# Performance work log

Measured on AMD Instinct MI355X. Metric: run time of the kernel, lower is better.

Reference implementation:

```python
import jax, jax.numpy as jnp
import numpy as np

N_NODES = 20000
N_EDGES = 320000
N_GRAPHS = 32
C = 256
L = 4
IN_DIM = 739
EDGE_DIM = 2 * C + 6
LN_EPS = 1e-5


def _layernorm(x, g, b):
    mu = jnp.mean(x, axis=-1, keepdims=True)
    var = jnp.mean(jnp.square(x - mu), axis=-1, keepdims=True)
    return (x - mu) * jax.lax.rsqrt(var + LN_EPS) * g + b


def setup_inputs() -> dict:
    key = jax.random.key(0)
    ks = jax.random.split(key, 20)
    d = {}
    d["x"] = jax.random.normal(ks[0], (N_NODES, IN_DIM), jnp.float32)
    d["x_pos"] = jax.random.normal(ks[1], (N_NODES, 3), jnp.float32)
    d["edge_index"] = jax.random.randint(ks[2], (2, N_EDGES), 0, N_NODES, jnp.int32)
    d["batch"] = jnp.sort(jax.random.randint(ks[3], (N_NODES,), 0, N_GRAPHS, jnp.int32))
    s = 0.02
    d["dense_w"] = jax.random.normal(ks[4], (IN_DIM, C), jnp.float32) * s
    d["dense_b"] = jnp.zeros((C,), jnp.float32)
    d["d1_w"] = jax.random.normal(ks[5], (L, C, C), jnp.float32) * s
    d["d1_b"] = jnp.zeros((L, C), jnp.float32)
    d["ln1_g"] = jnp.ones((L, EDGE_DIM), jnp.float32)
    d["ln1_b"] = jnp.zeros((L, EDGE_DIM), jnp.float32)
    d["w1_w"] = jax.random.normal(ks[6], (L, EDGE_DIM, 4), jnp.float32) * s
    d["w1_b"] = jnp.zeros((L, 4), jnp.float32)
    d["ln2_g"] = jnp.ones((L, 4), jnp.float32)
    d["ln2_b"] = jnp.zeros((L, 4), jnp.float32)
    d["w2_w"] = jax.random.normal(ks[7], (L, 4, 1), jnp.float32) * s
    d["w2_b"] = jnp.zeros((L, 1), jnp.float32)
    d["d2_w"] = jax.random.normal(ks[8], (L, C, C), jnp.float32) * s
    d["d2_b"] = jnp.zeros((L, C), jnp.float32)
    d["head_w"] = jax.random.normal(ks[9], (C, 1), jnp.float32) * s
    d["head_b"] = jnp.zeros((1,), jnp.float32)
    return d


def reference(x, x_pos, edge_index, batch, dense_w, dense_b, d1_w, d1_b,
              ln1_g, ln1_b, w1_w, w1_b, ln2_g, ln2_b, w2_w, w2_b,
              d2_w, d2_b, head_w, head_b):
    n = x.shape[0]
    src, dst = edge_index[0], edge_index[1]
    h = x @ dense_w + dense_b  # [N, C]
    for l in range(d1_w.shape[0]):
        # message: dense1 -> GELU (dropout is identity in eval)
        m = jax.nn.gelu(h @ d1_w[l] + d1_b[l], approximate=False)  # [N, C]
        sx = m[src]                                                # [E, C]
        # edge-MLP input: [src_x, dst_x, src_pos, dst_pos]
        e = jnp.concatenate([sx, m[dst], x_pos[src], x_pos[dst]], axis=-1)  # [E, 2C+6]
        e = _layernorm(e, ln1_g[l], ln1_b[l])
        e = jax.nn.gelu(e @ w1_w[l] + w1_b[l], approximate=False)  # [E, 4]
        e = _layernorm(e, ln2_g[l], ln2_b[l])
        w = jax.nn.sigmoid(e @ w2_w[l] + w2_b[l])                  # [E, 1]
        agg = jax.ops.segment_sum(sx * w, dst, num_segments=n)     # [N, C]
        # update: dense2 -> GELU
        h = jax.nn.gelu(agg @ d2_w[l] + d2_b[l], approximate=False)
    # global mean pool over graphs
    sums = jax.ops.segment_sum(h, batch, num_segments=N_GRAPHS)           # [G, C]
    cnts = jax.ops.segment_sum(jnp.ones((n, 1), h.dtype), batch, num_segments=N_GRAPHS)
    pooled = sums / jnp.maximum(cnts, 1.0)
    return pooled @ head_w + head_b  # [G, 1]
```

## Files before the change

kernel.cpp:

```cpp
#include <hip/hip_runtime.h>
#include <math.h>

#define N_NODES 20000
#define N_EDGES 320000
#define N_GRAPHS 32
#define CDIM 256
#define IN_DIMV 739
#define KPAD_DENSE 768
#define ED_DIM 518
#define NLAYERS 4
#define LN_EPS 1e-5f
#define SCAN_BLOCKS ((N_NODES + 255) / 256)

typedef _Float16 f16x8 __attribute__((ext_vector_type(8)));
typedef _Float16 f16x4 __attribute__((ext_vector_type(4)));
typedef float f32x4 __attribute__((ext_vector_type(4)));

__device__ __forceinline__ float gelu_exact(float x) {
    return 0.5f * x * (1.f + erff(x * 0.7071067811865475f));
}

__device__ __forceinline__ void gll16(const void* g, void* l) {
    __builtin_amdgcn_global_load_lds((const __attribute__((address_space(1))) void*)g,
                                     (__attribute__((address_space(3))) void*)l, 16, 0, 0);
}

__global__ __launch_bounds__(256)
void prep_all(const float* __restrict__ ln1_g, const float* __restrict__ ln1_b,
              const float* __restrict__ w1_w, float* __restrict__ cw,
              float* __restrict__ SgSb,
              const float* __restrict__ dense_w, _Float16* __restrict__ wt_dense,
              const float* __restrict__ d1_w, const float* __restrict__ d2_w,
              _Float16* __restrict__ wt_sq, int* __restrict__ deg,
              float* __restrict__ sdot,
              const float* __restrict__ x, _Float16* __restrict__ xh) {
    __shared__ float smem[2048 + 64];
    int b = blockIdx.x, tid = threadIdx.x;
    if (b < 79) {
        int i = b * 256 + tid;
        if (i < N_NODES) deg[i] = 0;
    } else if (b < 83) {
        int l = b - 79;
        float sg[4] = {0, 0, 0, 0}, sb[4] = {0, 0, 0, 0};
        for (int i = tid; i < ED_DIM; i += 256) {
            float g = ln1_g[l * ED_DIM + i];
            float bb = ln1_b[l * ED_DIM + i];
            float4 w = *(const float4*)&w1_w[(size_t)(l * ED_DIM + i) * 4];
            float4 c = make_float4(g * w.x, g * w.y, g * w.z, g * w.w);
            *(float4*)&cw[(size_t)(l * ED_DIM + i) * 4] = c;
            sg[0] += c.x; sg[1] += c.y; sg[2] += c.z; sg[3] += c.w;
            sb[0] += bb * w.x; sb[1] += bb * w.y; sb[2] += bb * w.z; sb[3] += bb * w.w;
        }
        for (int c = 0; c < 4; c++) { smem[tid * 8 + c] = sg[c]; smem[tid * 8 + 4 + c] = sb[c]; }
        __syncthreads();
        for (int s = 128; s > 0; s >>= 1) {
            if (tid < s)
                for (int c = 0; c < 8; c++) smem[tid * 8 + c] += smem[(tid + s) * 8 + c];
            __syncthreads();
        }
        if (tid < 8) SgSb[l * 8 + tid] = smem[tid];
    } else if (b < 275) {
        int q = b - 83;
        int kt = q >> 3, nt = q & 7;
        int i = tid >> 5, j = tid & 31;
        float* T = smem;
#pragma unroll
        for (int ii = 0; ii < 4; ii++) {
            int k = kt * 32 + i + ii * 8;
            T[(i + ii * 8) * 33 + j] = (k < IN_DIMV) ? dense_w[(size_t)k * 256 + nt * 32 + j] : 0.f;
        }
        __syncthreads();
#pragma unroll
        for (int ii = 0; ii < 4; ii++) {
            int n = nt * 32 + i + ii * 8;
            wt_dense[(size_t)n * KPAD_DENSE + kt * 32 + j] = (_Float16)T[j * 33 + i + ii * 8];
        }
    } else if (b < 787) {
        int q = b - 275;
        int z = q >> 6, kt = (q >> 3) & 7, nt = q & 7;
        const float* W = (z < 4) ? d1_w + (size_t)z * 65536 : d2_w + (size_t)(z - 4) * 65536;
        _Float16* O = wt_sq + (size_t)z * 65536;
        int i = tid >> 5, j = tid & 31;
        float* T = smem;
#pragma unroll
        for (int ii = 0; ii < 4; ii++)
            T[(i + ii * 8) * 33 + j] = W[(size_t)(kt * 32 + i + ii * 8) * 256 + nt * 32 + j];
        __syncthreads();
#pragma unroll
        for (int ii = 0; ii < 4; ii++)
            O[(size_t)(nt * 32 + i + ii * 8) * 256 + kt * 32 + j] = (_Float16)T[j * 33 + i + ii * 8];
    } else if (b < 866) {
        int i = (b - 787) * 256 + tid;
        if (i < N_NODES) sdot[i] = 0.f;
    } else {
        const int cb = b - 866;
        const int stride = 2048 * 256;
        const int nquads = (N_NODES * IN_DIMV) / 4;
        for (int q = cb * 256 + tid; q < nquads; q += stride) {
            float4 v = ((const float4*)x)[q];
            int base = q * 4;
            float vv[4] = {v.x, v.y, v.z, v.w};
#pragma unroll
            for (int e = 0; e < 4; ++e) {
                int idx = base + e;
                int row = idx / IN_DIMV;
                int col = idx - row * IN_DIMV;
                xh[row * KPAD_DENSE + col] = (_Float16)vv[e];
            }
        }
        const int npad = N_NODES * (KPAD_DENSE - IN_DIMV);
        for (int p = cb * 256 + tid; p < npad; p += stride) {
            int row = p / (KPAD_DENSE - IN_DIMV);
            int col = IN_DIMV + (p - row * (KPAD_DENSE - IN_DIMV));
            xh[row * KPAD_DENSE + col] = (_Float16)0.f;
        }
    }
}

__global__ void hist_gstart_kernel(const int* __restrict__ ei, const int* __restrict__ batch,
                                   int* __restrict__ deg, int* __restrict__ gstart) {
    int e = blockIdx.x * 256 + threadIdx.x;
    if (e < N_EDGES) atomicAdd(&deg[ei[N_EDGES + e]], 1);
    if (e < N_NODES) {
        int b = batch[e];
        int bprev = (e == 0) ? -1 : batch[e - 1];
        for (int g = bprev + 1; g <= b; g++) gstart[g] = e;
        if (e == N_NODES - 1)
            for (int g = b + 1; g <= N_GRAPHS; g++) gstart[g] = N_NODES;
    }
}

__global__ __launch_bounds__(256)
void scan1_kernel(const int* __restrict__ deg, int* __restrict__ bsum) {
    __shared__ int red[256];
    int t = threadIdx.x;
    int i = blockIdx.x * 256 + t;
    red[t] = (i < N_NODES) ? deg[i] : 0;
    __syncthreads();
    for (int s = 128; s > 0; s >>= 1) {
        if (t < s) red[t] += red[t + s];
        __syncthreads();
    }
    if (t == 0) bsum[blockIdx.x] = red[0];
}

__global__ __launch_bounds__(128)
void scan2_kernel(const int* __restrict__ bsum, int* __restrict__ boff) {
    __shared__ int s[128];
    int t = threadIdx.x;
    int v = (t < SCAN_BLOCKS) ? bsum[t] : 0;
    s[t] = v;
    __syncthreads();
    for (int off = 1; off < 128; off <<= 1) {
        int o = (t >= off) ? s[t - off] : 0;
        __syncthreads();
        s[t] += o;
        __syncthreads();
    }
    if (t < SCAN_BLOCKS) boff[t] = s[t] - v;
}

__global__ __launch_bounds__(256)
void scan3_kernel(const int* __restrict__ deg, const int* __restrict__ boff,
                  int* __restrict__ row_start, int* __restrict__ cursor) {
    __shared__ int s[256];
    int t = threadIdx.x;
    int i = blockIdx.x * 256 + t;
    int v = (i < N_NODES) ? deg[i] : 0;
    s[t] = v;
    __syncthreads();
    for (int off = 1; off < 256; off <<= 1) {
        int o = (t >= off) ? s[t - off] : 0;
        __syncthreads();
        s[t] += o;
        __syncthreads();
    }
    int base = boff[blockIdx.x];
    int excl = base + s[t] - v;
    if (i < N_NODES) {
        row_start[i] = excl;
        cursor[i] = excl;
    }
    if (i == N_NODES - 1) row_start[N_NODES] = base + s[t];
}

__global__ void scatter_kernel(const int* __restrict__ ei, int* __restrict__ cursor,
                               int* __restrict__ csr_src, int* __restrict__ slot) {
    int e = blockIdx.x * 256 + threadIdx.x;
    if (e < N_EDGES) {
        int d = ei[N_EDGES + e];
        int pos = atomicAdd(&cursor[d], 1);
        csr_src[pos] = ei[e];
        slot[e] = pos;
    }
}

template <int KSTEPS, int NBUF, bool GELU_ACT, bool DOT, bool SUMPART>
__global__ __launch_bounds__(256)
void gemm_v6(const _Float16* __restrict__ A, const _Float16* __restrict__ Bt,
             const float* __restrict__ bias, _Float16* __restrict__ C,
             const float* __restrict__ head_w, float* __restrict__ sdot,
             const float* __restrict__ cw, float* __restrict__ nsp) {
    constexpr int KDIM = KSTEPS * 64;
    __shared__ __align__(16) _Float16 Bs[NBUF * 128 * 64];
    __shared__ __align__(16) _Float16 As[NBUF * 64 * 64];

    const int tid = threadIdx.x;
    const int row0 = blockIdx.x * 64;
    const int col0 = blockIdx.y * 128;
    const int wave = tid >> 6, lane = tid & 63;
    const int quad = lane >> 4, lrow = lane & 15;
    const int wrow = wave >> 1, wcol = wave & 1;

    const int sr = tid >> 3;
    const int scb = (tid & 7) << 4;
    const int srcCb = scb ^ ((sr & 7) << 4);

    const char* bsrc[4];
#pragma unroll
    for (int i = 0; i < 4; ++i)
        bsrc[i] = (const char*)Bt + (size_t)(col0 + i * 32 + sr) * (KDIM * 2) + srcCb;
    char* const bdst = (char*)&Bs[0] + tid * 16;

    const char* asrc[2];
    char* const adst = (char*)&As[0] + tid * 16;
#pragma unroll
    for (int i = 0; i < 2; ++i) {
        int ar = row0 + i * 32 + sr;
        ar = (ar < N_NODES) ? ar : (N_NODES - 1);
        asrc[i] = (const char*)A + (size_t)ar * (KDIM * 2) + srcCb;
    }

    const int swz = ((lrow & 7) << 4) ^ (quad << 4);
    const int aro0 = (wrow * 32 + lrow) * 128;
    const int aro1 = aro0 + 2048;
    int bro[4];
#pragma unroll
    for (int t = 0; t < 4; ++t) bro[t] = (wcol * 64 + t * 16 + lrow) * 128;

    f32x4 acc[2][4];
#pragma unroll
    for (int i = 0; i < 2; ++i)
#pragma unroll
        for (int t = 0; t < 4; ++t) acc[i][t] = (f32x4){0.f, 0.f, 0.f, 0.f};

    auto stage = [&](int j) {
        const int kb = j * 128;
        const int b3 = (j % NBUF) * 16384;
        const int a3 = (j % NBUF) * 8192;
#pragma unroll
        for (int i = 0; i < 4; ++i) gll16(bsrc[i] + kb, bdst + b3 + i * 4096);
#pragma unroll
        for (int i = 0; i < 2; ++i) gll16(asrc[i] + kb, adst + a3 + i * 4096);
    };

    auto compute = [&](int k) {
        const char* pa = (const char*)&As[0] + (k % NBUF) * 8192;
        const char* pb = (const char*)&Bs[0] + (k % NBUF) * 16384;
        if constexpr (NBUF == 3) __builtin_amdgcn_s_setprio(1);
#pragma unroll
        for (int h = 0; h < 2; ++h) {
            const int cbs = (h << 6) ^ swz;
            f16x8 af0 = *(const f16x8*)(pa + aro0 + cbs);
            f16x8 af1 = *(const f16x8*)(pa + aro1 + cbs);
#pragma unroll
            for (int t = 0; t < 4; ++t) {
                f16x8 bf = *(const f16x8*)(pb + bro[t] + cbs);
                acc[0][t] = __builtin_amdgcn_mfma_f32_16x16x32_f16(af0, bf, acc[0][t], 0, 0, 0);
                acc[1][t] = __builtin_amdgcn_mfma_f32_16x16x32_f16(af1, bf, acc[1][t], 0, 0, 0);
            }
        }
        if constexpr (NBUF == 3) __builtin_amdgcn_s_setprio(0);
    };

    stage(0);
    if constexpr (NBUF == 3) {
        if (KSTEPS > 1) stage(1);
        asm volatile("s_waitcnt vmcnt(6)" ::: "memory");
        __builtin_amdgcn_sched_barrier(0);
        __builtin_amdgcn_s_barrier();
        __builtin_amdgcn_sched_barrier(0);
    } else {
        __syncthreads();
    }

#pragma unroll
    for (int k = 0; k < KSTEPS; ++k) {
        const int nxt = k + NBUF - 1;
        if (nxt < KSTEPS) stage(nxt);
        compute(k);
        if (k + 1 < KSTEPS) {
            if constexpr (NBUF == 3) {
                if (k + 2 < KSTEPS)
                    asm volatile("s_waitcnt vmcnt(6) lgkmcnt(0)" ::: "memory");
                else
                    asm volatile("s_waitcnt vmcnt(0) lgkmcnt(0)" ::: "memory");
                __builtin_amdgcn_sched_barrier(0);
                __builtin_amdgcn_s_barrier();
                __builtin_amdgcn_sched_barrier(0);
            } else {
                __syncthreads();
            }
        }
    }

    const int orow = row0 + wrow * 32 + quad * 4;
    const int ocolb = col0 + wcol * 64 + lrow;
    if constexpr (DOT) {
        float dp0[4] = {0.f, 0.f, 0.f, 0.f}, dp1[4] = {0.f, 0.f, 0.f, 0.f};
#pragma unroll
        for (int t = 0; t < 4; ++t) {
            const int col = ocolb + t * 16;
            const float hw = head_w[col];
            const float bv = bias[col];
#pragma unroll
            for (int r = 0; r < 4; ++r) {
                dp0[r] += gelu_exact(acc[0][t][r] + bv) * hw;
                dp1[r] += gelu_exact(acc[1][t][r] + bv) * hw;
            }
        }
#pragma unroll
        for (int r = 0; r < 4; ++r) {
#pragma unroll
            for (int off = 1; off < 16; off <<= 1) {
                dp0[r] += __shfl_xor(dp0[r], off, 64);
                dp1[r] += __shfl_xor(dp1[r], off, 64);
            }
        }
        if (lrow == 0) {
#pragma unroll
            for (int r = 0; r < 4; ++r) {
                if (orow + r < N_NODES) atomicAdd(&sdot[orow + r], dp0[r]);
                if (orow + 16 + r < N_NODES) atomicAdd(&sdot[orow + 16 + r], dp1[r]);
            }
        }
    } else if constexpr (SUMPART) {
        float4 c0v[4], c1v[4];
        float bv[4];
#pragma unroll
        for (int t = 0; t < 4; ++t) {
            const int col = ocolb + t * 16;
            c0v[t] = *(const float4*)&cw[(size_t)col * 4];
            c1v[t] = *(const float4*)&cw[(size_t)(256 + col) * 4];
            bv[t] = bias[col];
        }
        const int part = blockIdx.y * 2 + wcol;
        float* const npbase = nsp + (size_t)part * N_NODES * 12;
#pragma unroll
        for (int h = 0; h < 2; ++h) {
#pragma unroll
            for (int r = 0; r < 4; ++r) {
                const int row = orow + h * 16 + r;
                float p1x = 0.f, p1y = 0.f, p1z = 0.f, p1w = 0.f;
                float p2x = 0.f, p2y = 0.f, p2z = 0.f, p2w = 0.f;
                float q1 = 0.f, q2 = 0.f;
#pragma unroll
                for (int t = 0; t < 4; ++t) {
                    float v = gelu_exact(acc[h][t][r] + bv[t]);
                    _Float16 hv = (_Float16)v;
                    if (row < N_NODES) C[(size_t)row * 256 + (ocolb + t * 16)] = hv;
                    float av = (float)hv;
                    p1x += av * c0v[t].x; p1y += av * c0v[t].y;
                    p1z += av * c0v[t].z; p1w += av * c0v[t].w;
                    p2x += av * c1v[t].x; p2y += av * c1v[t].y;
                    p2z += av * c1v[t].z; p2w += av * c1v[t].w;
                    q1 += av; q2 += av * av;
                }
#pragma unroll
                for (int off = 1; off < 16; off <<= 1) {
                    p1x += __shfl_xor(p1x, off, 64); p1y += __shfl_xor(p1y, off, 64);
                    p1z += __shfl_xor(p1z, off, 64); p1w += __shfl_xor(p1w, off, 64);
                    p2x += __shfl_xor(p2x, off, 64); p2y += __shfl_xor(p2y, off, 64);
                    p2z += __shfl_xor(p2z, off, 64); p2w += __shfl_xor(p2w, off, 64);
                    q1 += __shfl_xor(q1, off, 64); q2 += __shfl_xor(q2, off, 64);
                }
                if (lrow == 0 && row < N_NODES) {
                    float* p = npbase + (size_t)row * 12;
                    *(float4*)p = make_float4(p1x, p1y, p1z, p1w);
                    *(float4*)(p + 4) = make_float4(p2x, p2y, p2z, p2w);
                    p[8] = q1;
                    p[9] = q2;
                }
            }
        }
    } else {
#pragma unroll
        for (int t = 0; t < 4; ++t) {
            const int col = ocolb + t * 16;
            const float bv = bias[col];
#pragma unroll
            for (int r = 0; r < 4; ++r) {
                float v0 = acc[0][t][r] + bv;
                float v1 = acc[1][t][r] + bv;
                if constexpr (GELU_ACT) { v0 = gelu_exact(v0); v1 = gelu_exact(v1); }
                if (orow + r < N_NODES)
                    C[(size_t)(orow + r) * 256 + col] = (_Float16)v0;
                if (orow + 16 + r < N_NODES)
                    C[(size_t)(orow + 16 + r) * 256 + col] = (_Float16)v1;
            }
        }
    }
}

__global__ __launch_bounds__(256)
void combine_ns_kernel(const float* __restrict__ nsp, float* __restrict__ ns) {
    int i = blockIdx.x * 256 + threadIdx.x;
    const int n4 = N_NODES * 3;
    if (i >= n4) return;
    float4 a = ((const float4*)nsp)[i];
    float4 b = ((const float4*)nsp)[i + n4];
    float4 c = ((const float4*)nsp)[i + 2 * n4];
    float4 d = ((const float4*)nsp)[i + 3 * n4];
    ((float4*)ns)[i] = make_float4(a.x + b.x + c.x + d.x, a.y + b.y + c.y + d.y,
                                   a.z + b.z + c.z + d.z, a.w + b.w + c.w + d.w);
}

__global__ __launch_bounds__(256)
void edge_weight_kernel(const float* __restrict__ ns, const float* __restrict__ x_pos,
                        const int* __restrict__ ei, const float* __restrict__ cw,
                        const float* __restrict__ SgSb, const float* __restrict__ w1_b,
                        const float* __restrict__ ln2_g, const float* __restrict__ ln2_b,
                        const float* __restrict__ w2_w, const float* __restrict__ w2_b,
                        const int* __restrict__ slot, float* __restrict__ w_csr) {
    int e = blockIdx.x * 256 + threadIdx.x;
    if (e >= N_EDGES) return;
    int s = ei[e], d = ei[N_EDGES + e];
    const float* nss = &ns[(size_t)s * 12];
    const float* nsd = &ns[(size_t)d * 12];
    float4 p1 = *(const float4*)nss;
    float4 p2 = *(const float4*)(nsd + 4);
    float S1 = nss[8] + nsd[8];
    float S2 = nss[9] + nsd[9];
    float D[4] = {p1.x + p2.x, p1.y + p2.y, p1.z + p2.z, p1.w + p2.w};
    float ps[6];
    ps[0] = x_pos[(size_t)s * 3 + 0];
    ps[1] = x_pos[(size_t)s * 3 + 1];
    ps[2] = x_pos[(size_t)s * 3 + 2];
    ps[3] = x_pos[(size_t)d * 3 + 0];
    ps[4] = x_pos[(size_t)d * 3 + 1];
    ps[5] = x_pos[(size_t)d * 3 + 2];
#pragma unroll
    for (int k = 0; k < 6; k++) {
        S1 += ps[k];
        S2 += ps[k] * ps[k];
        float4 c = *(const float4*)&cw[(size_t)(512 + k) * 4];
        D[0] += ps[k] * c.x; D[1] += ps[k] * c.y; D[2] += ps[k] * c.z; D[3] += ps[k] * c.w;
    }
    const float inv = 1.f / 518.f;
    float mu = S1 * inv;
    float var = fmaf(-mu, mu, S2 * inv);
    float rstd = rsqrtf(var + LN_EPS);
    float t[4];
#pragma unroll
    for (int c = 0; c < 4; c++)
        t[c] = gelu_exact(rstd * (D[c] - mu * SgSb[c]) + SgSb[4 + c] + w1_b[c]);
    float mu2 = 0.25f * (t[0] + t[1] + t[2] + t[3]);
    float var2 = 0.25f * ((t[0] - mu2) * (t[0] - mu2) + (t[1] - mu2) * (t[1] - mu2) +
                          (t[2] - mu2) * (t[2] - mu2) + (t[3] - mu2) * (t[3] - mu2));
    float r2 = rsqrtf(var2 + LN_EPS);
    float z = w2_b[0];
#pragma unroll
    for (int c = 0; c < 4; c++)
        z += ((t[c] - mu2) * r2 * ln2_g[c] + ln2_b[c]) * w2_w[c];
    w_csr[slot[e]] = 1.f / (1.f + expf(-z));
}

__global__ __launch_bounds__(256)
void agg_kernel(const _Float16* __restrict__ m, const int* __restrict__ csr_src,
                const float* __restrict__ w_csr, const int* __restrict__ row_start,
                _Float16* __restrict__ agg) {
    int n = blockIdx.x * 4 + (threadIdx.x >> 6);
    if (n >= N_NODES) return;
    int lane = threadIdx.x & 63;
    int beg = row_start[n], end = row_start[n + 1];
    float a0 = 0.f, a1 = 0.f, a2 = 0.f, a3 = 0.f;
    int j = beg;
    for (; j + 8 <= end; j += 8) {
        int si[8];
        float wi[8];
#pragma unroll
        for (int u = 0; u < 8; u++) { si[u] = csr_src[j + u]; wi[u] = w_csr[j + u]; }
        f16x4 v[8];
#pragma unroll
        for (int u = 0; u < 8; u++) v[u] = *(const f16x4*)&m[(size_t)si[u] * CDIM + lane * 4];
#pragma unroll
        for (int u = 0; u < 8; u++) {
            a0 = fmaf(wi[u], (float)v[u][0], a0);
            a1 = fmaf(wi[u], (float)v[u][1], a1);
            a2 = fmaf(wi[u], (float)v[u][2], a2);
            a3 = fmaf(wi[u], (float)v[u][3], a3);
        }
    }
    for (; j < end; j++) {
        int s = csr_src[j];
        float w = w_csr[j];
        f16x4 v = *(const f16x4*)&m[(size_t)s * CDIM + lane * 4];
        a0 = fmaf(w, (float)v[0], a0);
        a1 = fmaf(w, (float)v[1], a1);
        a2 = fmaf(w, (float)v[2], a2);
        a3 = fmaf(w, (float)v[3], a3);
    }
    f16x4 o;
    o[0] = (_Float16)a0; o[1] = (_Float16)a1; o[2] = (_Float16)a2; o[3] = (_Float16)a3;
    *(f16x4*)&agg[(size_t)n * CDIM + lane * 4] = o;
}

__global__ __launch_bounds__(256)
void final_head_kernel(const float* __restrict__ sdot, const int* __restrict__ gstart,
                       const float* __restrict__ head_b, float* __restrict__ out) {
    int g = blockIdx.x;
    int t = threadIdx.x;
    int beg = gstart[g], end = gstart[g + 1];
    float s = 0.f;
    for (int i = beg + t; i < end; i += 256) s += sdot[i];
    __shared__ float red[256];
    red[t] = s;
    __syncthreads();
    for (int k = 128; k > 0; k >>= 1) {
        if (t < k) red[t] += red[t + k];
        __syncthreads();
    }
    if (t == 0) out[g] = red[0] / fmaxf((float)(end - beg), 1.f) + head_b[0];
}

extern "C" void kernel_launch(void* const* d_in, const int* in_sizes, int n_in,
                              void* d_out, int out_size, void* d_ws, size_t ws_size,
                              hipStream_t stream) {
    const float* x       = (const float*)d_in[0];
    const float* x_pos   = (const float*)d_in[1];
    const int*   ei      = (const int*)d_in[2];
    const int*   batch   = (const int*)d_in[3];
    const float* dense_w = (const float*)d_in[4];
    const float* dense_b = (const float*)d_in[5];
    const float* d1_w    = (const float*)d_in[6];
    const float* d1_b    = (const float*)d_in[7];
    const float* ln1_g   = (const float*)d_in[8];
    const float* ln1_b   = (const float*)d_in[9];
    const float* w1_w    = (const float*)d_in[10];
    const float* w1_b    = (const float*)d_in[11];
    const float* ln2_g   = (const float*)d_in[12];
    const float* ln2_b   = (const float*)d_in[13];
    const float* w2_w    = (const float*)d_in[14];
    const float* w2_b    = (const float*)d_in[15];
    const float* d2_w    = (const float*)d_in[16];
    const float* d2_b    = (const float*)d_in[17];
    const float* head_w  = (const float*)d_in[18];
    const float* head_b  = (const float*)d_in[19];
    float* out = (float*)d_out;

    _Float16* hbuf0 = (_Float16*)d_ws;
    _Float16* hbuf1 = hbuf0 + (size_t)N_NODES * CDIM;
    _Float16* wt_dense = hbuf1 + (size_t)N_NODES * CDIM;
    _Float16* wt_sq    = wt_dense + (size_t)256 * KPAD_DENSE;
    _Float16* x_h      = wt_sq + (size_t)8 * 256 * 256;
    float* cw    = (float*)(x_h + (size_t)N_NODES * KPAD_DENSE);
    float* SgSb  = cw + (size_t)NLAYERS * ED_DIM * 4;
    float* ns    = SgSb + NLAYERS * 8;
    float* nsp   = ns + (size_t)N_NODES * 12;
    float* sdot  = nsp + (size_t)4 * N_NODES * 12;
    float* w_csr = sdot + N_NODES;
    int* gstart    = (int*)(w_csr + N_EDGES);
    int* deg       = gstart + N_GRAPHS + 1;
    int* row_start = deg + N_NODES;
    int* cursor    = row_start + N_NODES + 1;
    int* csr_src   = cursor + N_NODES;
    int* slot      = csr_src + N_EDGES;
    int* bsum      = slot + N_EDGES;
    int* boff      = bsum + SCAN_BLOCKS;

    prep_all<<<2914, 256, 0, stream>>>(ln1_g, ln1_b, w1_w, cw, SgSb,
                                       dense_w, wt_dense, d1_w, d2_w, wt_sq, deg,
                                       sdot, x, x_h);

    hist_gstart_kernel<<<(N_EDGES + 255) / 256, 256, 0, stream>>>(ei, batch, deg, gstart);
    scan1_kernel<<<SCAN_BLOCKS, 256, 0, stream>>>(deg, bsum);
    scan2_kernel<<<1, 128, 0, stream>>>(bsum, boff);
    scan3_kernel<<<SCAN_BLOCKS, 256, 0, stream>>>(deg, boff, row_start, cursor);
    scatter_kernel<<<(N_EDGES + 255) / 256, 256, 0, stream>>>(ei, cursor, csr_src, slot);

    const dim3 G2((N_NODES + 63) / 64, 2);
    gemm_v6<12, 3, false, false, false><<<G2, 256, 0, stream>>>(
        x_h, wt_dense, dense_b, hbuf0, nullptr, nullptr, nullptr, nullptr);

    _Float16* h = hbuf0;
    _Float16* other = hbuf1;
    for (int l = 0; l < NLAYERS; l++) {
        gemm_v6<4, 2, true, false, true><<<G2, 256, 0, stream>>>(
            h, wt_sq + (size_t)l * 65536, d1_b + l * CDIM, other, nullptr, nullptr,
            cw + (size_t)l * ED_DIM * 4, nsp);
        combine_ns_kernel<<<(N_NODES * 3 + 255) / 256, 256, 0, stream>>>(nsp, ns);
        edge_weight_kernel<<<(N_EDGES + 255) / 256, 256, 0, stream>>>(
            ns, x_pos, ei, cw + (size_t)l * ED_DIM * 4, SgSb + l * 8, w1_b + l * 4,
            ln2_g + l * 4, ln2_b + l * 4, w2_w + l * 4, w2_b + l, slot, w_csr);
        agg_kernel<<<(N_NODES + 3) / 4, 256, 0, stream>>>(other, csr_src, w_csr, row_start, h);
        if (l < NLAYERS - 1) {
            gemm_v6<4, 2, true, false, false><<<G2, 256, 0, stream>>>(
                h, wt_sq + (size_t)(4 + l) * 65536, d2_b + l * CDIM, other, nullptr, nullptr,
                nullptr, nullptr);
        } else {
            gemm_v6<4, 2, true, true, false><<<G2, 256, 0, stream>>>(
                h, wt_sq + (size_t)(4 + l) * 65536, d2_b + l * CDIM, other, head_w, sdot,
                nullptr, nullptr);
        }
        _Float16* tmp = h; h = other; other = tmp;
    }

    final_head_kernel<<<N_GRAPHS, 256, 0, stream>>>(sdot, gstart, head_b, out);
}
```

Measured before the change: 497.4 us.

## Fuse edge-weight computation into CSR aggregation kernel via wave shuffles

Merges the per-edge weight kernel into the per-destination aggregation kernel. Each wave computes the sigmoid edge weights for up to 64 incoming edges in parallel, one per lane, then broadcasts source index and weight with shuffles for the gather-accumulate. This drops the w_csr and slot buffers, the scattered weight write, one launch per layer, and the slot write in the scatter. In exchange the weight math is now serialized ahead of the gathers inside each wave, and lanes sit idle when a node has few edges (average degree is 16).

```diff
diff --git a/kernel.cpp b/kernel.cpp
--- a/kernel.cpp
+++ b/kernel.cpp
@@ -185,13 +185,12 @@
 }
 
 __global__ void scatter_kernel(const int* __restrict__ ei, int* __restrict__ cursor,
-                               int* __restrict__ csr_src, int* __restrict__ slot) {
+                               int* __restrict__ csr_src) {
     int e = blockIdx.x * 256 + threadIdx.x;
     if (e < N_EDGES) {
         int d = ei[N_EDGES + e];
         int pos = atomicAdd(&cursor[d], 1);
         csr_src[pos] = ei[e];
-        slot[e] = pos;
     }
 }
 
@@ -416,89 +415,109 @@
 }
 
 __global__ __launch_bounds__(256)
-void edge_weight_kernel(const float* __restrict__ ns, const float* __restrict__ x_pos,
-                        const int* __restrict__ ei, const float* __restrict__ cw,
-                        const float* __restrict__ SgSb, const float* __restrict__ w1_b,
-                        const float* __restrict__ ln2_g, const float* __restrict__ ln2_b,
-                        const float* __restrict__ w2_w, const float* __restrict__ w2_b,
-                        const int* __restrict__ slot, float* __restrict__ w_csr) {
-    int e = blockIdx.x * 256 + threadIdx.x;
-    if (e >= N_EDGES) return;
-    int s = ei[e], d = ei[N_EDGES + e];
-    const float* nss = &ns[(size_t)s * 12];
-    const float* nsd = &ns[(size_t)d * 12];
-    float4 p1 = *(const float4*)nss;
-    float4 p2 = *(const float4*)(nsd + 4);
-    float S1 = nss[8] + nsd[8];
-    float S2 = nss[9] + nsd[9];
-    float D[4] = {p1.x + p2.x, p1.y + p2.y, p1.z + p2.z, p1.w + p2.w};
-    float ps[6];
-    ps[0] = x_pos[(size_t)s * 3 + 0];
-    ps[1] = x_pos[(size_t)s * 3 + 1];
-    ps[2] = x_pos[(size_t)s * 3 + 2];
-    ps[3] = x_pos[(size_t)d * 3 + 0];
-    ps[4] = x_pos[(size_t)d * 3 + 1];
-    ps[5] = x_pos[(size_t)d * 3 + 2];
-#pragma unroll
-    for (int k = 0; k < 6; k++) {
-        S1 += ps[k];
-        S2 += ps[k] * ps[k];
-        float4 c = *(const float4*)&cw[(size_t)(512 + k) * 4];
-        D[0] += ps[k] * c.x; D[1] += ps[k] * c.y; D[2] += ps[k] * c.z; D[3] += ps[k] * c.w;
-    }
-    const float inv = 1.f / 518.f;
-    float mu = S1 * inv;
-    float var = fmaf(-mu, mu, S2 * inv);
-    float rstd = rsqrtf(var + LN_EPS);
-    float t[4];
-#pragma unroll
-    for (int c = 0; c < 4; c++)
-        t[c] = gelu_exact(rstd * (D[c] - mu * SgSb[c]) + SgSb[4 + c] + w1_b[c]);
-    float mu2 = 0.25f * (t[0] + t[1] + t[2] + t[3]);
-    float var2 = 0.25f * ((t[0] - mu2) * (t[0] - mu2) + (t[1] - mu2) * (t[1] - mu2) +
-                          (t[2] - mu2) * (t[2] - mu2) + (t[3] - mu2) * (t[3] - mu2));
-    float r2 = rsqrtf(var2 + LN_EPS);
-    float z = w2_b[0];
-#pragma unroll
-    for (int c = 0; c < 4; c++)
-        z += ((t[c] - mu2) * r2 * ln2_g[c] + ln2_b[c]) * w2_w[c];
-    w_csr[slot[e]] = 1.f / (1.f + expf(-z));
-}
-
-__global__ __launch_bounds__(256)
-void agg_kernel(const _Float16* __restrict__ m, const int* __restrict__ csr_src,
-                const float* __restrict__ w_csr, const int* __restrict__ row_start,
-                _Float16* __restrict__ agg) {
+void edge_agg_kernel(const _Float16* __restrict__ m, const int* __restrict__ csr_src,
+                     const int* __restrict__ row_start, const float* __restrict__ ns,
+                     const float* __restrict__ x_pos, const float* __restrict__ cw,
+                     const float* __restrict__ SgSb, const float* __restrict__ w1_b,
+                     const float* __restrict__ ln2_g, const float* __restrict__ ln2_b,
+                     const float* __restrict__ w2_w, const float* __restrict__ w2_b,
+                     _Float16* __restrict__ agg) {
     int n = blockIdx.x * 4 + (threadIdx.x >> 6);
     if (n >= N_NODES) return;
     int lane = threadIdx.x & 63;
+
+    const float* nsd = &ns[(size_t)n * 12];
+    float4 p2d = *(const float4*)(nsd + 4);
+    float nsd8 = nsd[8], nsd9 = nsd[9];
+    float pxn[3] = {x_pos[(size_t)n * 3 + 0], x_pos[(size_t)n * 3 + 1],
+                    x_pos[(size_t)n * 3 + 2]};
+    float4 cwp[6];
+#pragma unroll
+    for (int k = 0; k < 6; ++k) cwp[k] = *(const float4*)&cw[(size_t)(512 + k) * 4];
+    float sgv[8];
+#pragma unroll
+    for (int k = 0; k < 8; ++k) sgv[k] = SgSb[k];
+    float w1bv[4], l2g[4], l2b[4], w2wv[4];
+#pragma unroll
+    for (int k = 0; k < 4; ++k) {
+        w1bv[k] = w1_b[k]; l2g[k] = ln2_g[k]; l2b[k] = ln2_b[k]; w2wv[k] = w2_w[k];
+    }
+    const float w2bv = w2_b[0];
+
     int beg = row_start[n], end = row_start[n + 1];
     float a0 = 0.f, a1 = 0.f, a2 = 0.f, a3 = 0.f;
-    int j = beg;
-    for (; j + 8 <= end; j += 8) {
-        int si[8];
-        float wi[8];
-#pragma unroll
-        for (int u = 0; u < 8; u++) { si[u] = csr_src[j + u]; wi[u] = w_csr[j + u]; }
-        f16x4 v[8];
-#pragma unroll
-        for (int u = 0; u < 8; u++) v[u] = *(const f16x4*)&m[(size_t)si[u] * CDIM + lane * 4];
-#pragma unroll
-        for (int u = 0; u < 8; u++) {
-            a0 = fmaf(wi[u], (float)v[u][0], a0);
-            a1 = fmaf(wi[u], (float)v[u][1], a1);
-            a2 = fmaf(wi[u], (float)v[u][2], a2);
-            a3 = fmaf(wi[u], (float)v[u][3], a3);
-        }
-    }
-    for (; j < end; j++) {
-        int s = csr_src[j];
-        float w = w_csr[j];
-        f16x4 v = *(const f16x4*)&m[(size_t)s * CDIM + lane * 4];
-        a0 = fmaf(w, (float)v[0], a0);
-        a1 = fmaf(w, (float)v[1], a1);
-        a2 = fmaf(w, (float)v[2], a2);
-        a3 = fmaf(w, (float)v[3], a3);
+
+    for (int cb = beg; cb < end; cb += 64) {
+        int cnt = min(64, end - cb);
+        float w = 0.f;
+        int s = 0;
+        if (lane < cnt) {
+            s = csr_src[cb + lane];
+            const float* nss = &ns[(size_t)s * 12];
+            float4 p1 = *(const float4*)nss;
+            float S1 = nss[8] + nsd8;
+            float S2 = nss[9] + nsd9;
+            float D[4] = {p1.x + p2d.x, p1.y + p2d.y, p1.z + p2d.z, p1.w + p2d.w};
+            float ps[6];
+            ps[0] = x_pos[(size_t)s * 3 + 0];
+            ps[1] = x_pos[(size_t)s * 3 + 1];
+            ps[2] = x_pos[(size_t)s * 3 + 2];
+            ps[3] = pxn[0]; ps[4] = pxn[1]; ps[5] = pxn[2];
+#pragma unroll
+            for (int k = 0; k < 6; ++k) {
+                S1 += ps[k];
+                S2 += ps[k] * ps[k];
+                D[0] += ps[k] * cwp[k].x; D[1] += ps[k] * cwp[k].y;
+                D[2] += ps[k] * cwp[k].z; D[3] += ps[k] * cwp[k].w;
+            }
+            const float inv = 1.f / 518.f;
+            float mu = S1 * inv;
+            float var = fmaf(-mu, mu, S2 * inv);
+            float rstd = rsqrtf(var + LN_EPS);
+            float t[4];
+#pragma unroll
+            for (int c = 0; c < 4; ++c)
+                t[c] = gelu_exact(rstd * (D[c] - mu * sgv[c]) + sgv[4 + c] + w1bv[c]);
+            float mu2 = 0.25f * (t[0] + t[1] + t[2] + t[3]);
+            float var2 = 0.25f * ((t[0] - mu2) * (t[0] - mu2) + (t[1] - mu2) * (t[1] - mu2) +
+                                  (t[2] - mu2) * (t[2] - mu2) + (t[3] - mu2) * (t[3] - mu2));
+            float r2 = rsqrtf(var2 + LN_EPS);
+            float z = w2bv;
+#pragma unroll
+            for (int c = 0; c < 4; ++c)
+                z += ((t[c] - mu2) * r2 * l2g[c] + l2b[c]) * w2wv[c];
+            w = 1.f / (1.f + expf(-z));
+        }
+        int u = 0;
+        for (; u + 8 <= cnt; u += 8) {
+            int si[8];
+            float wi[8];
+#pragma unroll
+            for (int uu = 0; uu < 8; ++uu) {
+                si[uu] = __shfl(s, u + uu, 64);
+                wi[uu] = __shfl(w, u + uu, 64);
+            }
+            f16x4 v[8];
+#pragma unroll
+            for (int uu = 0; uu < 8; ++uu)
+                v[uu] = *(const f16x4*)&m[(size_t)si[uu] * CDIM + lane * 4];
+#pragma unroll
+            for (int uu = 0; uu < 8; ++uu) {
+                a0 = fmaf(wi[uu], (float)v[uu][0], a0);
+                a1 = fmaf(wi[uu], (float)v[uu][1], a1);
+                a2 = fmaf(wi[uu], (float)v[uu][2], a2);
+                a3 = fmaf(wi[uu], (float)v[uu][3], a3);
+            }
+        }
+        for (; u < cnt; ++u) {
+            int si = __shfl(s, u, 64);
+            float wi = __shfl(w, u, 64);
+            f16x4 v = *(const f16x4*)&m[(size_t)si * CDIM + lane * 4];
+            a0 = fmaf(wi, (float)v[0], a0);
+            a1 = fmaf(wi, (float)v[1], a1);
+            a2 = fmaf(wi, (float)v[2], a2);
+            a3 = fmaf(wi, (float)v[3], a3);
+        }
     }
     f16x4 o;
     o[0] = (_Float16)a0; o[1] = (_Float16)a1; o[2] = (_Float16)a2; o[3] = (_Float16)a3;
@@ -558,14 +577,12 @@
     float* ns    = SgSb + NLAYERS * 8;
     float* nsp   = ns + (size_t)N_NODES * 12;
     float* sdot  = nsp + (size_t)4 * N_NODES * 12;
-    float* w_csr = sdot + N_NODES;
-    int* gstart    = (int*)(w_csr + N_EDGES);
+    int* gstart    = (int*)(sdot + N_NODES);
     int* deg       = gstart + N_GRAPHS + 1;
     int* row_start = deg + N_NODES;
     int* cursor    = row_start + N_NODES + 1;
     int* csr_src   = cursor + N_NODES;
-    int* slot      = csr_src + N_EDGES;
-    int* bsum      = slot + N_EDGES;
+    int* bsum      = csr_src + N_EDGES;
     int* boff      = bsum + SCAN_BLOCKS;
 
     prep_all<<<2914, 256, 0, stream>>>(ln1_g, ln1_b, w1_w, cw, SgSb,
@@ -576,7 +593,7 @@
     scan1_kernel<<<SCAN_BLOCKS, 256, 0, stream>>>(deg, bsum);
     scan2_kernel<<<1, 128, 0, stream>>>(bsum, boff);
     scan3_kernel<<<SCAN_BLOCKS, 256, 0, stream>>>(deg, boff, row_start, cursor);
-    scatter_kernel<<<(N_EDGES + 255) / 256, 256, 0, stream>>>(ei, cursor, csr_src, slot);
+    scatter_kernel<<<(N_EDGES + 255) / 256, 256, 0, stream>>>(ei, cursor, csr_src);
 
     const dim3 G2((N_NODES + 63) / 64, 2);
     gemm_v6<12, 3, false, false, false><<<G2, 256, 0, stream>>>(
@@ -589,10 +606,10 @@
             h, wt_sq + (size_t)l * 65536, d1_b + l * CDIM, other, nullptr, nullptr,
             cw + (size_t)l * ED_DIM * 4, nsp);
         combine_ns_kernel<<<(N_NODES * 3 + 255) / 256, 256, 0, stream>>>(nsp, ns);
-        edge_weight_kernel<<<(N_EDGES + 255) / 256, 256, 0, stream>>>(
-            ns, x_pos, ei, cw + (size_t)l * ED_DIM * 4, SgSb + l * 8, w1_b + l * 4,
-            ln2_g + l * 4, ln2_b + l * 4, w2_w + l * 4, w2_b + l, slot, w_csr);
-        agg_kernel<<<(N_NODES + 3) / 4, 256, 0, stream>>>(other, csr_src, w_csr, row_start, h);
+        edge_agg_kernel<<<(N_NODES + 3) / 4, 256, 0, stream>>>(
+            other, csr_src, row_start, ns, x_pos, cw + (size_t)l * ED_DIM * 4,
+            SgSb + l * 8, w1_b + l * 4, ln2_g + l * 4, ln2_b + l * 4,
+            w2_w + l * 4, w2_b + l, h);
         if (l < NLAYERS - 1) {
             gemm_v6<4, 2, true, false, false><<<G2, 256, 0, stream>>>(
                 h, wt_sq + (size_t)(4 + l) * 65536, d2_b + l * CDIM, other, nullptr, nullptr,
```

Result: faster. 472.1 us, median of 4 (-5.1%).
